# Kernel tuning notes

Hardware: AMD Instinct MI355X
Metric: run time of the kernel (lower is better)

## Reference

```python
import jax, jax.numpy as jnp
import numpy as np

BN_EPS = 1e-5


def _square_distance(src, dst):
    # src: (B,N,3), dst: (B,S,3) -> (B,N,S) squared euclidean distance
    d = -2.0 * jnp.einsum('bnc,bsc->bns', src, dst)
    d += jnp.sum(src * src, -1)[:, :, None]
    d += jnp.sum(dst * dst, -1)[:, None, :]
    return d


def _bn_relu(x, gamma, beta):
    # training-mode BatchNorm1d over (B, C, N): stats over (B, N)
    mean = jnp.mean(x, axis=(0, 2), keepdims=True)
    var = jnp.var(x, axis=(0, 2), keepdims=True)  # biased, as torch uses for normalization
    xhat = (x - mean) * jax.lax.rsqrt(var + BN_EPS)
    return jax.nn.relu(xhat * gamma[None, :, None] + beta[None, :, None])


def setup_inputs() -> dict:
    key = jax.random.key(0)
    ks = jax.random.split(key, 8)
    B, N, S, C1, C2 = 4, 8192, 2048, 128, 256
    inp = {
        'xyz1': jax.random.normal(ks[0], (B, 3, N), jnp.float32),
        'xyz2': jax.random.normal(ks[1], (B, 3, S), jnp.float32),
        'points1': jax.random.normal(ks[2], (B, C1, N), jnp.float32),
        'points2': jax.random.normal(ks[3], (B, C2, S), jnp.float32),
        'w0': jax.random.normal(ks[4], (256, C1 + C2), jnp.float32) * (1.0 / np.sqrt(C1 + C2)),
        'b0': jnp.zeros((256,), jnp.float32),
        'gamma0': jnp.ones((256,), jnp.float32),
        'beta0': jnp.zeros((256,), jnp.float32),
        'w1': jax.random.normal(ks[5], (128, 256), jnp.float32) * (1.0 / np.sqrt(256)),
        'b1': jnp.zeros((128,), jnp.float32),
        'gamma1': jnp.ones((128,), jnp.float32),
        'beta1': jnp.zeros((128,), jnp.float32),
    }
    return inp


def reference(xyz1, xyz2, points1, points2, w0, b0, gamma0, beta0, w1, b1, gamma1, beta1):
    B, _, N = xyz1.shape
    S = xyz2.shape[2]
    xyz1_t = jnp.transpose(xyz1, (0, 2, 1))  # (B,N,3)
    xyz2_t = jnp.transpose(xyz2, (0, 2, 1))  # (B,S,3)
    dist = _square_distance(xyz1_t, xyz2_t)  # (B,N,S)
    neg_d3, idx = jax.lax.top_k(-dist, 3)    # 3 smallest distances
    d3 = -neg_d3                             # (B,N,3)
    dist_recip = 1.0 / (d3 + 1e-8)
    weight = dist_recip / jnp.sum(dist_recip, axis=2, keepdims=True)  # (B,N,3)
    points2_t = jnp.transpose(points2, (0, 2, 1))  # (B,S,C2)
    bidx = jnp.arange(B)[:, None, None]
    neighbor = points2_t[bidx, idx]                 # (B,N,3,C2)
    interp = jnp.sum(neighbor * weight[..., None], axis=2)  # (B,N,C2)
    interp = jnp.transpose(interp, (0, 2, 1))               # (B,C2,N)
    x = jnp.concatenate([points1, interp], axis=1)          # (B,C1+C2,N)
    x = _bn_relu(jnp.einsum('oc,bcn->bon', w0, x) + b0[None, :, None], gamma0, beta0)
    x = _bn_relu(jnp.einsum('oc,bcn->bon', w1, x) + b1[None, :, None], gamma1, beta1)
    return x
```

## Files before the change

### kernel.cpp

```cpp
#include <hip/hip_runtime.h>
#include <hip/hip_bf16.h>

#define BATCH 4
#define NPTS  8192
#define SPTS  2048
#define C1    128
#define C2    256
#define CIN   384
#define H0    256
#define H1    128
#define NSLICE 32

typedef __attribute__((ext_vector_type(8))) short bf16x8;
typedef __attribute__((ext_vector_type(4))) float f32x4;

__device__ __forceinline__ unsigned short f2bf(float x) {
  union { float f; unsigned u; } v; v.f = x;
  unsigned r = v.u + 0x7fff + ((v.u >> 16) & 1);
  return (unsigned short)(r >> 16);
}
__device__ __forceinline__ float bf2f(unsigned short u) {
  union { unsigned u; float f; } v; v.u = ((unsigned)u) << 16; return v.f;
}

__global__ __launch_bounds__(256) void prep_kernel(
    const float* __restrict__ p2, unsigned short* __restrict__ p2tb,
    const float* __restrict__ xyz2, float4* __restrict__ xp,
    const float* __restrict__ w0, const float* __restrict__ w1,
    unsigned short* __restrict__ Wp,
    const float* __restrict__ p1, unsigned short* __restrict__ Xp,
    float* __restrict__ stats) {
  __shared__ unsigned short shmem[64 * 136];
  int bid = blockIdx.x;
  int t = threadIdx.x;

  if (bid < 512) {
    int b = bid >> 7, rem = bid & 127;
    int s0 = (rem >> 2) * 64, c0 = (rem & 3) * 64;
    const float* src = p2 + (size_t)b * C2 * SPTS;
    int ss = t & 63, cseg = t >> 6;
#pragma unroll
    for (int i = 0; i < 16; i++) {
      int cc = cseg + i * 4;
      shmem[ss * 72 + cc] = f2bf(src[(size_t)(c0 + cc) * SPTS + s0 + ss]);
    }
    __syncthreads();
    int s = t >> 2, chunk = t & 3;
    uint4 v0 = *(const uint4*)&shmem[s * 72 + chunk * 16];
    uint4 v1 = *(const uint4*)&shmem[s * 72 + chunk * 16 + 8];
    unsigned short* dst = p2tb + (size_t)b * SPTS * C2 + (size_t)(s0 + s) * C2 + c0 + chunk * 16;
    *(uint4*)dst = v0;
    *(uint4*)(dst + 8) = v1;
  } else if (bid < 1024) {
    int b2 = bid - 512;
    int b = b2 >> 7, n0 = (b2 & 127) * 64;
    int nn = t & 63, c4 = t >> 6;
#pragma unroll
    for (int i = 0; i < 32; i++) {
      int c = i * 4 + c4;
      shmem[nn * 136 + c] = f2bf(p1[((size_t)b * C1 + c) * NPTS + n0 + nn]);
    }
    __syncthreads();
    int n = t >> 2;
#pragma unroll
    for (int j = 0; j < 4; j++) {
      int ch = (t & 3) + j * 4;
      uint4 v = *(const uint4*)&shmem[n * 136 + ch * 8];
      *(uint4*)&Xp[((size_t)b * NPTS + n0 + n) * CIN + ch * 8] = v;
    }
  } else if (bid < 1056) {
    int idx = (bid - 1024) * 256 + t;
    int b = idx >> 11, s = idx & (SPTS - 1);
    const float* x2 = xyz2 + (size_t)b * 3 * SPTS;
    float x = x2[s], y = x2[SPTS + s], z = x2[2 * SPTS + s];
    xp[idx] = make_float4(-2.f * x, -2.f * y, -2.f * z, x * x + y * y + z * z);
  } else if (bid < 1184) {
    int idx = ((bid - 1056) * 256 + t) * 4;
    const float* src = (idx < H0 * CIN) ? (w0 + idx) : (w1 + (idx - H0 * CIN));
    float4 v = *(const float4*)src;
    ushort4 o;
    o.x = f2bf(v.x); o.y = f2bf(v.y); o.z = f2bf(v.z); o.w = f2bf(v.w);
    *(ushort4*)(Wp + idx) = o;
  } else {
    int i4 = ((bid - 1184) * 256 + t) * 4;
    if (i4 < NSLICE * 768) *(float4*)(stats + i4) = make_float4(0.f, 0.f, 0.f, 0.f);
  }
}

#define INS3(d, s, e0, e1, e2, j0, j1, j2)                        \
  {                                                               \
    bool lt0 = (d) < (e0), lt1 = (d) < (e1), lt2 = (d) < (e2);    \
    j2 = lt1 ? (j1) : (lt2 ? (s) : (j2));                         \
    j1 = lt0 ? (j0) : (lt1 ? (s) : (j1));                         \
    j0 = lt0 ? (s) : (j0);                                        \
    e2 = __builtin_amdgcn_fmed3f((d), (e1), (e2));                \
    e1 = __builtin_amdgcn_fmed3f((d), (e0), (e1));                \
    e0 = fminf((d), (e0));                                        \
  }

__global__ __launch_bounds__(1024) void knn_interp_kernel(
    const float* __restrict__ xyz1, const float4* __restrict__ xp,
    const unsigned short* __restrict__ p2tb, unsigned short* __restrict__ Xp) {
  int b = blockIdx.y;
  int t = threadIdx.x;
  int lane = t & 63;
  int w = __builtin_amdgcn_readfirstlane(t >> 6);
  int n = blockIdx.x * 64 + lane;
  const float* x1 = xyz1 + (size_t)b * 3 * NPTS;
  float px = x1[n], py = x1[NPTS + n], pz = x1[2 * NPTS + n];

  const int CHUNK = SPTS / 16;
  int sbase = w * CHUNK;
  const float4* cp = xp + (size_t)b * SPTS + sbase;

  float d0 = 3e38f, d1 = 3e38f, d2 = 3e38f;
  int i0 = 0, i1 = 0, i2 = 0;
#pragma unroll 8
  for (int j = 0; j < CHUNK; j++) {
    float4 c = cp[j];
    float d = fmaf(c.z, pz, fmaf(c.y, py, fmaf(c.x, px, c.w)));
    int s = sbase + j;
    INS3(d, s, d0, d1, d2, i0, i1, i2);
  }

  __shared__ float dsh[16][64][3];
  __shared__ int   ish[16][64][3];
  __shared__ int   widx[64][3];
  __shared__ float wwgt[64][3];
  dsh[w][lane][0] = d0; dsh[w][lane][1] = d1; dsh[w][lane][2] = d2;
  ish[w][lane][0] = i0; ish[w][lane][1] = i1; ish[w][lane][2] = i2;
  __syncthreads();

  if (t < 256) {
    int g = t >> 6, q = t & 63;
    float e0 = 3e38f, e1 = 3e38f, e2 = 3e38f;
    int j0 = 0, j1 = 0, j2 = 0;
#pragma unroll
    for (int c = 0; c < 4; c++) {
#pragma unroll
      for (int k = 0; k < 3; k++) {
        float d = dsh[4 * g + c][q][k];
        int s = ish[4 * g + c][q][k];
        INS3(d, s, e0, e1, e2, j0, j1, j2);
      }
    }
    dsh[4 * g][q][0] = e0; dsh[4 * g][q][1] = e1; dsh[4 * g][q][2] = e2;
    ish[4 * g][q][0] = j0; ish[4 * g][q][1] = j1; ish[4 * g][q][2] = j2;
  }
  __syncthreads();

  if (t < 64) {
    float e0 = 3e38f, e1 = 3e38f, e2 = 3e38f;
    int j0 = 0, j1 = 0, j2 = 0;
#pragma unroll
    for (int c = 0; c < 4; c++) {
#pragma unroll
      for (int k = 0; k < 3; k++) {
        float d = dsh[4 * c][t][k];
        int s = ish[4 * c][t][k];
        INS3(d, s, e0, e1, e2, j0, j1, j2);
      }
    }
    float qq = fmaf(px, px, fmaf(py, py, pz * pz));
    float r0 = 1.f / (e0 + qq + 1e-8f);
    float r1 = 1.f / (e1 + qq + 1e-8f);
    float r2 = 1.f / (e2 + qq + 1e-8f);
    float rs = 1.f / (r0 + r1 + r2);
    widx[t][0] = j0; widx[t][1] = j1; widx[t][2] = j2;
    wwgt[t][0] = r0 * rs; wwgt[t][1] = r1 * rs; wwgt[t][2] = r2 * rs;
  }
  __syncthreads();

  const unsigned short* base = p2tb + (size_t)b * SPTS * C2;
  int c2 = (t & 127) * 2;
  int psub = t >> 7;
  unsigned short* xrow = Xp + ((size_t)b * NPTS + blockIdx.x * 64) * CIN + C1 + c2;
#pragma unroll
  for (int i = 0; i < 8; i++) {
    int pl = psub + i * 8;
    int g0 = widx[pl][0], g1 = widx[pl][1], g2 = widx[pl][2];
    float w0v = wwgt[pl][0], w1v = wwgt[pl][1], w2v = wwgt[pl][2];
    unsigned a0 = *(const unsigned*)(base + (size_t)g0 * C2 + c2);
    unsigned a1 = *(const unsigned*)(base + (size_t)g1 * C2 + c2);
    unsigned a2 = *(const unsigned*)(base + (size_t)g2 * C2 + c2);
    float v0 = w0v * bf2f((unsigned short)a0) + w1v * bf2f((unsigned short)a1) +
               w2v * bf2f((unsigned short)a2);
    float v1 = w0v * bf2f((unsigned short)(a0 >> 16)) + w1v * bf2f((unsigned short)(a1 >> 16)) +
               w2v * bf2f((unsigned short)(a2 >> 16));
    unsigned pk = (unsigned)f2bf(v0) | ((unsigned)f2bf(v1) << 16);
    *(unsigned*)(xrow + (size_t)pl * CIN) = pk;
  }
}

__global__ __launch_bounds__(256) void gemm0_kernel(
    const unsigned short* __restrict__ A, const unsigned short* __restrict__ X,
    const float* __restrict__ bias, unsigned short* __restrict__ Y0,
    float* __restrict__ stats) {
  constexpr int KD = CIN;
  __shared__ unsigned short lds[24576];
  int b = blockIdx.z;
  int n0 = blockIdx.x * 128;
  int o0 = blockIdx.y * 128;
  int t = threadIdx.x;
  int lane = t & 63;
  int w = __builtin_amdgcn_readfirstlane(t >> 6);
  int mhalf = (w & 1) * 64, nhalf = (w >> 1) * 64;
  const unsigned short* Xb = X + (size_t)b * NPTS * KD;
  int rA = lane >> 2;
  int cofs = (lane & 3) * 8;

  auto stage = [&](int buf, int k0) {
#pragma unroll
    for (int q = 0; q < 2; q++) {
      int r0 = w * 32 + q * 16;
      const unsigned short* ga = A + (size_t)(o0 + r0 + rA) * KD + k0 + cofs;
      __builtin_amdgcn_global_load_lds(
          (const __attribute__((address_space(1))) void*)ga,
          (__attribute__((address_space(3))) void*)(lds + buf * 4096 + r0 * 32), 16, 0, 0);
      const unsigned short* gb = Xb + (size_t)(n0 + r0 + rA) * KD + k0 + cofs;
      __builtin_amdgcn_global_load_lds(
          (const __attribute__((address_space(1))) void*)gb,
          (__attribute__((address_space(3))) void*)(lds + 12288 + buf * 4096 + r0 * 32), 16, 0, 0);
    }
  };

  constexpr int NT = KD / 32;
  f32x4 acc[4][4] = {};
  int mi = lane & 15, kq = (lane >> 4) * 8;

  stage(0, 0);
  stage(1, 32);

#pragma unroll
  for (int kt = 0; kt < NT; ++kt) {
    if (kt < NT - 1) asm volatile("s_waitcnt vmcnt(4)" ::: "memory");
    else             asm volatile("s_waitcnt vmcnt(0)" ::: "memory");
    __builtin_amdgcn_s_barrier();
    asm volatile("" ::: "memory");
    __builtin_amdgcn_sched_barrier(0);

    if (kt + 2 < NT) stage((kt + 2) % 3, (kt + 2) * 32);

    const unsigned short* Ac = lds + (kt % 3) * 4096;
    const unsigned short* Bc = lds + 12288 + (kt % 3) * 4096;
    bf16x8 af[4], bfr[4];
#pragma unroll
    for (int i = 0; i < 4; i++) {
      af[i]  = *(const bf16x8*)(Ac + (mhalf + i * 16 + mi) * 32 + kq);
      bfr[i] = *(const bf16x8*)(Bc + (nhalf + i * 16 + mi) * 32 + kq);
    }
#pragma unroll
    for (int mt = 0; mt < 4; mt++)
#pragma unroll
      for (int nt = 0; nt < 4; nt++)
        acc[mt][nt] = __builtin_amdgcn_mfma_f32_16x16x32_bf16(
            af[mt], bfr[nt], acc[mt][nt], 0, 0, 0);
  }

  __syncthreads();

  int slice = ((blockIdx.x << 2) + blockIdx.z) & (NSLICE - 1);
  float* sb = stats + slice * 768;
  float* qb = stats + slice * 768 + 256;

  int rq = (lane >> 4) * 4;
#pragma unroll
  for (int mt = 0; mt < 4; mt++) {
#pragma unroll
    for (int r = 0; r < 4; r++) {
      int ml = mhalf + mt * 16 + rq + r;
      float bv = bias[o0 + ml];
      float ps = 0.f, pq = 0.f;
#pragma unroll
      for (int nt = 0; nt < 4; nt++) {
        int nl = nhalf + nt * 16 + mi;
        float v = acc[mt][nt][r] + bv;
        ps += v; pq += v * v;
        lds[nl * 136 + ml] = f2bf(v);
      }
#pragma unroll
      for (int off = 1; off < 16; off <<= 1) {
        ps += __shfl_xor(ps, off, 16);
        pq += __shfl_xor(pq, off, 16);
      }
      if (mi == 0) {
        atomicAdd(&sb[o0 + ml], ps);
        atomicAdd(&qb[o0 + ml], pq);
      }
    }
  }
  __syncthreads();

  int row = t >> 1, ch0 = (t & 1) * 64;
  unsigned short* Yr = Y0 + ((size_t)b * NPTS + n0 + row) * H0 + o0 + ch0;
#pragma unroll
  for (int j = 0; j < 8; j++) {
    uint4 v = *(const uint4*)&lds[row * 136 + ch0 + j * 8];
    *(uint4*)(Yr + j * 8) = v;
  }
}

__global__ __launch_bounds__(256) void gemm1_kernel(
    const unsigned short* __restrict__ A, const unsigned short* __restrict__ Y0,
    const float* __restrict__ bias, float* __restrict__ out,
    float* __restrict__ stats, const float* __restrict__ gamma0,
    const float* __restrict__ beta0) {
  constexpr int KD = H0;
  __shared__ unsigned short As[2][4096];
  __shared__ unsigned short Bs[2][4096];
  __shared__ float aS[256], sS[256];
  int b = blockIdx.z;
  int n0 = blockIdx.x * 128;
  int t = threadIdx.x;
  int lane = t & 63;
  int w = __builtin_amdgcn_readfirstlane(t >> 6);
  int mhalf = (w & 1) * 64, nhalf = (w >> 1) * 64;
  int rA = lane >> 2;
  int cofs = (lane & 3) * 8;
  const unsigned short* Yb = Y0 + ((size_t)b * NPTS + n0) * KD;

  {
    float ms = 0.f, vs = 0.f;
#pragma unroll 8
    for (int sl = 0; sl < NSLICE; sl++) {
      ms += stats[sl * 768 + t];
      vs += stats[sl * 768 + 256 + t];
    }
    const float inv = 1.f / (float)(BATCH * NPTS);
    float mean = ms * inv;
    float var = vs * inv - mean * mean;
    float ia = gamma0[t] * rsqrtf(var + 1e-5f);
    aS[t] = ia; sS[t] = beta0[t] - mean * ia;
  }
  __syncthreads();

  auto stageA = [&](int buf, int k0) {
#pragma unroll
    for (int q = 0; q < 2; q++) {
      int r0 = w * 32 + q * 16;
      const unsigned short* ga = A + (size_t)(r0 + rA) * KD + k0 + cofs;
      __builtin_amdgcn_global_load_lds(
          (const __attribute__((address_space(1))) void*)ga,
          (__attribute__((address_space(3))) void*)(&As[buf][r0 * 32]), 16, 0, 0);
    }
  };
  bf16x8 br[2];
  auto loadB = [&](int k0) {
#pragma unroll
    for (int q = 0; q < 2; q++) {
      int r0 = w * 32 + q * 16;
      br[q] = *(const bf16x8*)(Yb + (size_t)(r0 + rA) * KD + k0 + cofs);
    }
  };
  auto writeB = [&](int buf, int k0) {
#pragma unroll
    for (int q = 0; q < 2; q++) {
      int r0 = w * 32 + q * 16;
      bf16x8 v = br[q], o;
#pragma unroll
      for (int e = 0; e < 8; e++) {
        float f = bf2f((unsigned short)v[e]);
        f = fmaxf(fmaf(f, aS[k0 + cofs + e], sS[k0 + cofs + e]), 0.f);
        o[e] = (short)f2bf(f);
      }
      *(bf16x8*)(&Bs[buf][(r0 + rA) * 32 + cofs]) = o;
    }
  };

  constexpr int NT = KD / 32;
  f32x4 acc[4][4] = {};
  int mi = lane & 15, kq = (lane >> 4) * 8;

  stageA(0, 0);
  loadB(0);
  int buf = 0;
#pragma unroll
  for (int kt = 0; kt < NT; ++kt) {
    asm volatile("s_waitcnt vmcnt(0)" ::: "memory");
    __builtin_amdgcn_sched_barrier(0);
    writeB(buf, kt * 32);
    asm volatile("s_waitcnt lgkmcnt(0)" ::: "memory");
    asm volatile("s_barrier" ::: "memory");
    __builtin_amdgcn_sched_barrier(0);
    if (kt + 1 < NT) { stageA(buf ^ 1, (kt + 1) * 32); loadB((kt + 1) * 32); }

    bf16x8 af[4], bfr[4];
#pragma unroll
    for (int i = 0; i < 4; i++) {
      af[i]  = *(const bf16x8*)(&As[buf][(mhalf + i * 16 + mi) * 32 + kq]);
      bfr[i] = *(const bf16x8*)(&Bs[buf][(nhalf + i * 16 + mi) * 32 + kq]);
    }
#pragma unroll
    for (int mt = 0; mt < 4; mt++)
#pragma unroll
      for (int nt = 0; nt < 4; nt++)
        acc[mt][nt] = __builtin_amdgcn_mfma_f32_16x16x32_bf16(
            af[mt], bfr[nt], acc[mt][nt], 0, 0, 0);
    buf ^= 1;
  }

  int slice = ((blockIdx.x << 2) + blockIdx.z) & (NSLICE - 1);
  float* sb = stats + slice * 768 + 512;
  float* qb = stats + slice * 768 + 640;
  float* Yo = out + (size_t)b * H1 * NPTS;

  int rq = (lane >> 4) * 4;
#pragma unroll
  for (int mt = 0; mt < 4; mt++) {
#pragma unroll
    for (int r = 0; r < 4; r++) {
      int m = mhalf + mt * 16 + rq + r;
      float bv = bias[m];
      float ps = 0.f, pq = 0.f;
#pragma unroll
      for (int nt = 0; nt < 4; nt++) {
        int n = n0 + nhalf + nt * 16 + mi;
        float v = acc[mt][nt][r] + bv;
        ps += v; pq += v * v;
        Yo[(size_t)m * NPTS + n] = v;
      }
#pragma unroll
      for (int off = 1; off < 16; off <<= 1) {
        ps += __shfl_xor(ps, off, 16);
        pq += __shfl_xor(pq, off, 16);
      }
      if (mi == 0) {
        atomicAdd(&sb[m], ps);
        atomicAdd(&qb[m], pq);
      }
    }
  }
}

__global__ __launch_bounds__(256) void bn_apply_kernel(
    float* __restrict__ Y, const float* __restrict__ stats,
    const float* __restrict__ gamma, const float* __restrict__ beta) {
  __shared__ float sh2[2];
  int idx0 = blockIdx.x * 1024;
  int c = (idx0 >> 13) & (H1 - 1);
  int t = threadIdx.x;
  if (t < 32) {
    float ms = stats[t * 768 + 512 + c];
    float vs = stats[t * 768 + 640 + c];
#pragma unroll
    for (int off = 16; off > 0; off >>= 1) {
      ms += __shfl_down(ms, off, 32);
      vs += __shfl_down(vs, off, 32);
    }
    if (t == 0) {
      const float inv = 1.f / (float)(BATCH * NPTS);
      float mean = ms * inv;
      float var = vs * inv - mean * mean;
      float ia = gamma[c] * rsqrtf(var + 1e-5f);
      sh2[0] = ia; sh2[1] = beta[c] - mean * ia;
    }
  }
  __syncthreads();
  float ia = sh2[0], sh = sh2[1];
  int i = idx0 + t * 4;
  float4 v = *(float4*)(Y + i);
  v.x = fmaxf(v.x * ia + sh, 0.f);
  v.y = fmaxf(v.y * ia + sh, 0.f);
  v.z = fmaxf(v.z * ia + sh, 0.f);
  v.w = fmaxf(v.w * ia + sh, 0.f);
  *(float4*)(Y + i) = v;
}

extern "C" void kernel_launch(void* const* d_in, const int* in_sizes, int n_in,
                              void* d_out, int out_size, void* d_ws, size_t ws_size,
                              hipStream_t stream) {
  const float* xyz1    = (const float*)d_in[0];
  const float* xyz2    = (const float*)d_in[1];
  const float* points1 = (const float*)d_in[2];
  const float* points2 = (const float*)d_in[3];
  const float* w0      = (const float*)d_in[4];
  const float* b0      = (const float*)d_in[5];
  const float* gamma0  = (const float*)d_in[6];
  const float* beta0   = (const float*)d_in[7];
  const float* w1      = (const float*)d_in[8];
  const float* b1      = (const float*)d_in[9];
  const float* gamma1  = (const float*)d_in[10];
  const float* beta1   = (const float*)d_in[11];
  float* out = (float*)d_out;

  char* ws = (char*)d_ws;
  unsigned short* p2tb = (unsigned short*)ws;  ws += (size_t)BATCH * SPTS * C2 * 2;
  unsigned short* Xp = (unsigned short*)ws;    ws += (size_t)BATCH * NPTS * CIN * 2;
  unsigned short* Y0 = (unsigned short*)ws;    ws += (size_t)BATCH * NPTS * H0 * 2;
  unsigned short* Wp = (unsigned short*)ws;    ws += (size_t)(H0 * CIN + H1 * H0) * 2;
  float4* xyz2p = (float4*)(((uintptr_t)ws + 15) & ~(uintptr_t)15);
  ws = (char*)xyz2p + (size_t)BATCH * SPTS * 16;
  float* stats = (float*)ws;                   ws += (size_t)NSLICE * 768 * 4;
  (void)ws_size; (void)in_sizes; (void)n_in; (void)out_size;

  prep_kernel<<<dim3(1208), 256, 0, stream>>>(points2, p2tb, xyz2, xyz2p,
                                              w0, w1, Wp, points1, Xp, stats);
  knn_interp_kernel<<<dim3(NPTS / 64, BATCH), 1024, 0, stream>>>(xyz1, xyz2p, p2tb, Xp);
  gemm0_kernel<<<dim3(NPTS / 128, H0 / 128, BATCH), 256, 0, stream>>>(
      Wp, Xp, b0, Y0, stats);
  gemm1_kernel<<<dim3(NPTS / 128, 1, BATCH), 256, 0, stream>>>(
      Wp + H0 * CIN, Y0, b1, out, stats, gamma0, beta0);
  bn_apply_kernel<<<dim3(BATCH * H1 * NPTS / 1024), 256, 0, stream>>>(
      out, stats, gamma1, beta1);
}
```

Before: 180.8 us.

## Fuse both MLP GEMMs and BN passes into one persistent kernel with grid barriers

The gemm0, gemm1 and bn_apply kernels are replaced by a single persistent kernel of 256 blocks. Each block computes all 256 layer-0 channels for its 128 points and keeps them in LDS instead of writing Y0 to global memory. It then waits at a grid barrier for the BN0 statistics, runs the second GEMM from LDS, and waits at a second grid barrier before applying BN1 and ReLU in registers before the final store. This removes the Y0 round trip, the separate BN pass over the output, and two launches. In exchange it depends on all 256 blocks being co-resident, does atomic spin-waits, reads W1 straight from global memory, and uses fewer blocks than before, which lowers parallelism.

New measurement: 218.8 us. 1.21x slower.

```diff
diff --git a/kernel.cpp b/kernel.cpp
--- a/kernel.cpp
+++ b/kernel.cpp
@@ -10,6 +10,7 @@
 #define H0    256
 #define H1    128
 #define NSLICE 32
+#define GRID_MLP 256
 
 typedef __attribute__((ext_vector_type(8))) short bf16x8;
 typedef __attribute__((ext_vector_type(4))) float f32x4;
@@ -21,6 +22,17 @@
 }
 __device__ __forceinline__ float bf2f(unsigned short u) {
   union { unsigned u; float f; } v; v.u = ((unsigned)u) << 16; return v.f;
+}
+
+__device__ __forceinline__ void grid_barrier(int* bar, int target) {
+  __syncthreads();
+  if (threadIdx.x == 0) {
+    __threadfence();
+    __hip_atomic_fetch_add(bar, 1, __ATOMIC_RELEASE, __HIP_MEMORY_SCOPE_AGENT);
+    while (__hip_atomic_load(bar, __ATOMIC_ACQUIRE, __HIP_MEMORY_SCOPE_AGENT) < target)
+      __builtin_amdgcn_s_sleep(2);
+  }
+  __syncthreads();
 }
 
 __global__ __launch_bounds__(256) void prep_kernel(
@@ -83,7 +95,7 @@
     *(ushort4*)(Wp + idx) = o;
   } else {
     int i4 = ((bid - 1184) * 256 + t) * 4;
-    if (i4 < NSLICE * 768) *(float4*)(stats + i4) = make_float4(0.f, 0.f, 0.f, 0.f);
+    if (i4 < NSLICE * 768 + 16) *(float4*)(stats + i4) = make_float4(0.f, 0.f, 0.f, 0.f);
   }
 }
 
@@ -192,278 +204,228 @@
   }
 }
 
-__global__ __launch_bounds__(256) void gemm0_kernel(
-    const unsigned short* __restrict__ A, const unsigned short* __restrict__ X,
-    const float* __restrict__ bias, unsigned short* __restrict__ Y0,
-    float* __restrict__ stats) {
-  constexpr int KD = CIN;
-  __shared__ unsigned short lds[24576];
-  int b = blockIdx.z;
-  int n0 = blockIdx.x * 128;
-  int o0 = blockIdx.y * 128;
+__global__ __launch_bounds__(256, 1) void fused_mlp_kernel(
+    const unsigned short* __restrict__ Wp, const unsigned short* __restrict__ Xp,
+    const float* __restrict__ bias0, const float* __restrict__ g0,
+    const float* __restrict__ be0, const float* __restrict__ bias1,
+    const float* __restrict__ g1, const float* __restrict__ be1,
+    float* __restrict__ out, float* __restrict__ stats) {
+  __shared__ unsigned short lds[36864];
+  __shared__ float aS0[256], sS0[256], aS1[128], sS1[128];
+  int* gbar = (int*)(stats + NSLICE * 768);
+
+  int bid = blockIdx.x;
+  int b = bid >> 6;
+  int n0 = (bid & 63) * 128;
   int t = threadIdx.x;
   int lane = t & 63;
   int w = __builtin_amdgcn_readfirstlane(t >> 6);
-  int mhalf = (w & 1) * 64, nhalf = (w >> 1) * 64;
-  const unsigned short* Xb = X + (size_t)b * NPTS * KD;
+  int mi = lane & 15, kq = (lane >> 4) * 8;
+  int rq = (lane >> 4) * 4;
   int rA = lane >> 2;
   int cofs = (lane & 3) * 8;
+  int slice = bid & (NSLICE - 1);
+
+  int mq = (w & 1) * 128;
+  int nh = (w >> 1) * 64;
+  const unsigned short* Xb = Xp + ((size_t)b * NPTS + n0) * CIN;
 
   auto stage = [&](int buf, int k0) {
+    unsigned short* dstA = lds + buf * 12288;
+    unsigned short* dstB = dstA + 8192;
+#pragma unroll
+    for (int q = 0; q < 4; q++) {
+      int r0 = w * 64 + q * 16;
+      const unsigned short* ga = Wp + (size_t)(r0 + rA) * CIN + k0 + cofs;
+      __builtin_amdgcn_global_load_lds(
+          (const __attribute__((address_space(1))) void*)ga,
+          (__attribute__((address_space(3))) void*)(dstA + r0 * 32), 16, 0, 0);
+    }
 #pragma unroll
     for (int q = 0; q < 2; q++) {
       int r0 = w * 32 + q * 16;
-      const unsigned short* ga = A + (size_t)(o0 + r0 + rA) * KD + k0 + cofs;
-      __builtin_amdgcn_global_load_lds(
-          (const __attribute__((address_space(1))) void*)ga,
-          (__attribute__((address_space(3))) void*)(lds + buf * 4096 + r0 * 32), 16, 0, 0);
-      const unsigned short* gb = Xb + (size_t)(n0 + r0 + rA) * KD + k0 + cofs;
+      const unsigned short* gb = Xb + (size_t)(r0 + rA) * CIN + k0 + cofs;
       __builtin_amdgcn_global_load_lds(
           (const __attribute__((address_space(1))) void*)gb,
-          (__attribute__((address_space(3))) void*)(lds + 12288 + buf * 4096 + r0 * 32), 16, 0, 0);
+          (__attribute__((address_space(3))) void*)(dstB + r0 * 32), 16, 0, 0);
     }
   };
 
-  constexpr int NT = KD / 32;
-  f32x4 acc[4][4] = {};
-  int mi = lane & 15, kq = (lane >> 4) * 8;
+  constexpr int NT0 = CIN / 32;
+  f32x4 acc[8][4] = {};
 
   stage(0, 0);
   stage(1, 32);
 
 #pragma unroll
-  for (int kt = 0; kt < NT; ++kt) {
-    if (kt < NT - 1) asm volatile("s_waitcnt vmcnt(4)" ::: "memory");
-    else             asm volatile("s_waitcnt vmcnt(0)" ::: "memory");
+  for (int kt = 0; kt < NT0; ++kt) {
+    if (kt < NT0 - 1) asm volatile("s_waitcnt vmcnt(6)" ::: "memory");
+    else              asm volatile("s_waitcnt vmcnt(0)" ::: "memory");
     __builtin_amdgcn_s_barrier();
     asm volatile("" ::: "memory");
     __builtin_amdgcn_sched_barrier(0);
 
-    if (kt + 2 < NT) stage((kt + 2) % 3, (kt + 2) * 32);
-
-    const unsigned short* Ac = lds + (kt % 3) * 4096;
-    const unsigned short* Bc = lds + 12288 + (kt % 3) * 4096;
-    bf16x8 af[4], bfr[4];
-#pragma unroll
-    for (int i = 0; i < 4; i++) {
-      af[i]  = *(const bf16x8*)(Ac + (mhalf + i * 16 + mi) * 32 + kq);
-      bfr[i] = *(const bf16x8*)(Bc + (nhalf + i * 16 + mi) * 32 + kq);
-    }
-#pragma unroll
-    for (int mt = 0; mt < 4; mt++)
-#pragma unroll
-      for (int nt = 0; nt < 4; nt++)
-        acc[mt][nt] = __builtin_amdgcn_mfma_f32_16x16x32_bf16(
-            af[mt], bfr[nt], acc[mt][nt], 0, 0, 0);
-  }
-
-  __syncthreads();
-
-  int slice = ((blockIdx.x << 2) + blockIdx.z) & (NSLICE - 1);
-  float* sb = stats + slice * 768;
-  float* qb = stats + slice * 768 + 256;
-
-  int rq = (lane >> 4) * 4;
-#pragma unroll
-  for (int mt = 0; mt < 4; mt++) {
-#pragma unroll
-    for (int r = 0; r < 4; r++) {
-      int ml = mhalf + mt * 16 + rq + r;
-      float bv = bias[o0 + ml];
-      float ps = 0.f, pq = 0.f;
-#pragma unroll
-      for (int nt = 0; nt < 4; nt++) {
-        int nl = nhalf + nt * 16 + mi;
-        float v = acc[mt][nt][r] + bv;
-        ps += v; pq += v * v;
-        lds[nl * 136 + ml] = f2bf(v);
-      }
-#pragma unroll
-      for (int off = 1; off < 16; off <<= 1) {
-        ps += __shfl_xor(ps, off, 16);
-        pq += __shfl_xor(pq, off, 16);
-      }
-      if (mi == 0) {
-        atomicAdd(&sb[o0 + ml], ps);
-        atomicAdd(&qb[o0 + ml], pq);
-      }
-    }
-  }
-  __syncthreads();
-
-  int row = t >> 1, ch0 = (t & 1) * 64;
-  unsigned short* Yr = Y0 + ((size_t)b * NPTS + n0 + row) * H0 + o0 + ch0;
-#pragma unroll
-  for (int j = 0; j < 8; j++) {
-    uint4 v = *(const uint4*)&lds[row * 136 + ch0 + j * 8];
-    *(uint4*)(Yr + j * 8) = v;
-  }
-}
-
-__global__ __launch_bounds__(256) void gemm1_kernel(
-    const unsigned short* __restrict__ A, const unsigned short* __restrict__ Y0,
-    const float* __restrict__ bias, float* __restrict__ out,
-    float* __restrict__ stats, const float* __restrict__ gamma0,
-    const float* __restrict__ beta0) {
-  constexpr int KD = H0;
-  __shared__ unsigned short As[2][4096];
-  __shared__ unsigned short Bs[2][4096];
-  __shared__ float aS[256], sS[256];
-  int b = blockIdx.z;
-  int n0 = blockIdx.x * 128;
-  int t = threadIdx.x;
-  int lane = t & 63;
-  int w = __builtin_amdgcn_readfirstlane(t >> 6);
-  int mhalf = (w & 1) * 64, nhalf = (w >> 1) * 64;
-  int rA = lane >> 2;
-  int cofs = (lane & 3) * 8;
-  const unsigned short* Yb = Y0 + ((size_t)b * NPTS + n0) * KD;
+    if (kt + 2 < NT0) stage((kt + 2) % 3, (kt + 2) * 32);
+
+    const unsigned short* Ac = lds + (kt % 3) * 12288;
+    const unsigned short* Bc = Ac + 8192;
+    bf16x8 af[8], bfr[4];
+#pragma unroll
+    for (int i = 0; i < 8; i++)
+      af[i] = *(const bf16x8*)(Ac + (mq + i * 16 + mi) * 32 + kq);
+#pragma unroll
+    for (int j = 0; j < 4; j++)
+      bfr[j] = *(const bf16x8*)(Bc + (nh + j * 16 + mi) * 32 + kq);
+#pragma unroll
+    for (int i = 0; i < 8; i++)
+#pragma unroll
+      for (int j = 0; j < 4; j++)
+        acc[i][j] = __builtin_amdgcn_mfma_f32_16x16x32_bf16(
+            af[i], bfr[j], acc[i][j], 0, 0, 0);
+  }
+
+  __syncthreads();
+  unsigned short* yt = lds;
+  {
+    float* sb = stats + slice * 768;
+    float* qb = sb + 256;
+#pragma unroll
+    for (int i = 0; i < 8; i++) {
+#pragma unroll
+      for (int rp = 0; rp < 2; rp++) {
+        int m0 = mq + i * 16 + rq + rp * 2;
+        float bva = bias0[m0], bvb = bias0[m0 + 1];
+        float psA = 0.f, pqA = 0.f, psB = 0.f, pqB = 0.f;
+#pragma unroll
+        for (int j = 0; j < 4; j++) {
+          int n = nh + j * 16 + mi;
+          float va = acc[i][j][rp * 2] + bva;
+          float vb = acc[i][j][rp * 2 + 1] + bvb;
+          psA += va; pqA += va * va; psB += vb; pqB += vb * vb;
+          *(unsigned*)&yt[n * 264 + m0] = (unsigned)f2bf(va) | ((unsigned)f2bf(vb) << 16);
+        }
+#pragma unroll
+        for (int off = 1; off < 16; off <<= 1) {
+          psA += __shfl_xor(psA, off, 16); pqA += __shfl_xor(pqA, off, 16);
+          psB += __shfl_xor(psB, off, 16); pqB += __shfl_xor(pqB, off, 16);
+        }
+        if (mi == 0) {
+          atomicAdd(&sb[m0], psA); atomicAdd(&qb[m0], pqA);
+          atomicAdd(&sb[m0 + 1], psB); atomicAdd(&qb[m0 + 1], pqB);
+        }
+      }
+    }
+  }
+  grid_barrier(gbar, GRID_MLP);
 
   {
     float ms = 0.f, vs = 0.f;
-#pragma unroll 8
+#pragma unroll 4
     for (int sl = 0; sl < NSLICE; sl++) {
-      ms += stats[sl * 768 + t];
-      vs += stats[sl * 768 + 256 + t];
+      ms += __hip_atomic_load(&stats[sl * 768 + t], __ATOMIC_RELAXED, __HIP_MEMORY_SCOPE_AGENT);
+      vs += __hip_atomic_load(&stats[sl * 768 + 256 + t], __ATOMIC_RELAXED, __HIP_MEMORY_SCOPE_AGENT);
     }
     const float inv = 1.f / (float)(BATCH * NPTS);
     float mean = ms * inv;
     float var = vs * inv - mean * mean;
-    float ia = gamma0[t] * rsqrtf(var + 1e-5f);
-    aS[t] = ia; sS[t] = beta0[t] - mean * ia;
-  }
-  __syncthreads();
-
-  auto stageA = [&](int buf, int k0) {
-#pragma unroll
-    for (int q = 0; q < 2; q++) {
-      int r0 = w * 32 + q * 16;
-      const unsigned short* ga = A + (size_t)(r0 + rA) * KD + k0 + cofs;
-      __builtin_amdgcn_global_load_lds(
-          (const __attribute__((address_space(1))) void*)ga,
-          (__attribute__((address_space(3))) void*)(&As[buf][r0 * 32]), 16, 0, 0);
-    }
-  };
-  bf16x8 br[2];
-  auto loadB = [&](int k0) {
-#pragma unroll
-    for (int q = 0; q < 2; q++) {
-      int r0 = w * 32 + q * 16;
-      br[q] = *(const bf16x8*)(Yb + (size_t)(r0 + rA) * KD + k0 + cofs);
-    }
-  };
-  auto writeB = [&](int buf, int k0) {
-#pragma unroll
-    for (int q = 0; q < 2; q++) {
-      int r0 = w * 32 + q * 16;
-      bf16x8 v = br[q], o;
+    float ia = g0[t] * rsqrtf(var + 1e-5f);
+    aS0[t] = ia; sS0[t] = be0[t] - mean * ia;
+  }
+  __syncthreads();
+  {
+    int row = t >> 1, c0 = (t & 1) * 128;
+#pragma unroll
+    for (int jj = 0; jj < 16; jj++) {
+      bf16x8 v = *(bf16x8*)&yt[row * 264 + c0 + jj * 8];
+      bf16x8 o;
 #pragma unroll
       for (int e = 0; e < 8; e++) {
-        float f = bf2f((unsigned short)v[e]);
-        f = fmaxf(fmaf(f, aS[k0 + cofs + e], sS[k0 + cofs + e]), 0.f);
+        int ch = c0 + jj * 8 + e;
+        float f = fmaxf(fmaf(bf2f((unsigned short)v[e]), aS0[ch], sS0[ch]), 0.f);
         o[e] = (short)f2bf(f);
       }
-      *(bf16x8*)(&Bs[buf][(r0 + rA) * 32 + cofs]) = o;
-    }
-  };
-
-  constexpr int NT = KD / 32;
-  f32x4 acc[4][4] = {};
-  int mi = lane & 15, kq = (lane >> 4) * 8;
-
-  stageA(0, 0);
-  loadB(0);
-  int buf = 0;
-#pragma unroll
-  for (int kt = 0; kt < NT; ++kt) {
-    asm volatile("s_waitcnt vmcnt(0)" ::: "memory");
-    __builtin_amdgcn_sched_barrier(0);
-    writeB(buf, kt * 32);
-    asm volatile("s_waitcnt lgkmcnt(0)" ::: "memory");
-    asm volatile("s_barrier" ::: "memory");
-    __builtin_amdgcn_sched_barrier(0);
-    if (kt + 1 < NT) { stageA(buf ^ 1, (kt + 1) * 32); loadB((kt + 1) * 32); }
-
-    bf16x8 af[4], bfr[4];
+      *(bf16x8*)&yt[row * 264 + c0 + jj * 8] = o;
+    }
+  }
+  __syncthreads();
+
+  int mh1 = (w & 1) * 64, nh1 = (w >> 1) * 64;
+  const unsigned short* W1 = Wp + H0 * CIN;
+  f32x4 acc1[4][4] = {};
+#pragma unroll
+  for (int kt = 0; kt < H0 / 32; kt++) {
+    bf16x8 a1[4], b1f[4];
+#pragma unroll
+    for (int i = 0; i < 4; i++)
+      a1[i] = *(const bf16x8*)(W1 + (size_t)(mh1 + i * 16 + mi) * H0 + kt * 32 + kq);
+#pragma unroll
+    for (int j = 0; j < 4; j++)
+      b1f[j] = *(const bf16x8*)&yt[(nh1 + j * 16 + mi) * 264 + kt * 32 + kq];
+#pragma unroll
+    for (int i = 0; i < 4; i++)
+#pragma unroll
+      for (int j = 0; j < 4; j++)
+        acc1[i][j] = __builtin_amdgcn_mfma_f32_16x16x32_bf16(
+            a1[i], b1f[j], acc1[i][j], 0, 0, 0);
+  }
+
+  {
+    float* sb = stats + slice * 768 + 512;
+    float* qb = sb + 128;
 #pragma unroll
     for (int i = 0; i < 4; i++) {
-      af[i]  = *(const bf16x8*)(&As[buf][(mhalf + i * 16 + mi) * 32 + kq]);
-      bfr[i] = *(const bf16x8*)(&Bs[buf][(nhalf + i * 16 + mi) * 32 + kq]);
-    }
-#pragma unroll
-    for (int mt = 0; mt < 4; mt++)
-#pragma unroll
-      for (int nt = 0; nt < 4; nt++)
-        acc[mt][nt] = __builtin_amdgcn_mfma_f32_16x16x32_bf16(
-            af[mt], bfr[nt], acc[mt][nt], 0, 0, 0);
-    buf ^= 1;
-  }
-
-  int slice = ((blockIdx.x << 2) + blockIdx.z) & (NSLICE - 1);
-  float* sb = stats + slice * 768 + 512;
-  float* qb = stats + slice * 768 + 640;
-  float* Yo = out + (size_t)b * H1 * NPTS;
-
-  int rq = (lane >> 4) * 4;
-#pragma unroll
-  for (int mt = 0; mt < 4; mt++) {
-#pragma unroll
-    for (int r = 0; r < 4; r++) {
-      int m = mhalf + mt * 16 + rq + r;
-      float bv = bias[m];
-      float ps = 0.f, pq = 0.f;
-#pragma unroll
-      for (int nt = 0; nt < 4; nt++) {
-        int n = n0 + nhalf + nt * 16 + mi;
-        float v = acc[mt][nt][r] + bv;
-        ps += v; pq += v * v;
-        Yo[(size_t)m * NPTS + n] = v;
-      }
-#pragma unroll
-      for (int off = 1; off < 16; off <<= 1) {
-        ps += __shfl_xor(ps, off, 16);
-        pq += __shfl_xor(pq, off, 16);
-      }
-      if (mi == 0) {
-        atomicAdd(&sb[m], ps);
-        atomicAdd(&qb[m], pq);
-      }
-    }
-  }
-}
-
-__global__ __launch_bounds__(256) void bn_apply_kernel(
-    float* __restrict__ Y, const float* __restrict__ stats,
-    const float* __restrict__ gamma, const float* __restrict__ beta) {
-  __shared__ float sh2[2];
-  int idx0 = blockIdx.x * 1024;
-  int c = (idx0 >> 13) & (H1 - 1);
-  int t = threadIdx.x;
-  if (t < 32) {
-    float ms = stats[t * 768 + 512 + c];
-    float vs = stats[t * 768 + 640 + c];
-#pragma unroll
-    for (int off = 16; off > 0; off >>= 1) {
-      ms += __shfl_down(ms, off, 32);
-      vs += __shfl_down(vs, off, 32);
-    }
-    if (t == 0) {
-      const float inv = 1.f / (float)(BATCH * NPTS);
-      float mean = ms * inv;
-      float var = vs * inv - mean * mean;
-      float ia = gamma[c] * rsqrtf(var + 1e-5f);
-      sh2[0] = ia; sh2[1] = beta[c] - mean * ia;
-    }
-  }
-  __syncthreads();
-  float ia = sh2[0], sh = sh2[1];
-  int i = idx0 + t * 4;
-  float4 v = *(float4*)(Y + i);
-  v.x = fmaxf(v.x * ia + sh, 0.f);
-  v.y = fmaxf(v.y * ia + sh, 0.f);
-  v.z = fmaxf(v.z * ia + sh, 0.f);
-  v.w = fmaxf(v.w * ia + sh, 0.f);
-  *(float4*)(Y + i) = v;
+#pragma unroll
+      for (int r = 0; r < 4; r++) {
+        int m = mh1 + i * 16 + rq + r;
+        float bv = bias1[m];
+        float ps = 0.f, pq = 0.f;
+#pragma unroll
+        for (int j = 0; j < 4; j++) {
+          float v = acc1[i][j][r] + bv;
+          acc1[i][j][r] = v;
+          ps += v; pq += v * v;
+        }
+#pragma unroll
+        for (int off = 1; off < 16; off <<= 1) {
+          ps += __shfl_xor(ps, off, 16);
+          pq += __shfl_xor(pq, off, 16);
+        }
+        if (mi == 0) { atomicAdd(&sb[m], ps); atomicAdd(&qb[m], pq); }
+      }
+    }
+  }
+  grid_barrier(gbar, 2 * GRID_MLP);
+
+  if (t < 128) {
+    float ms = 0.f, vs = 0.f;
+#pragma unroll 4
+    for (int sl = 0; sl < NSLICE; sl++) {
+      ms += __hip_atomic_load(&stats[sl * 768 + 512 + t], __ATOMIC_RELAXED, __HIP_MEMORY_SCOPE_AGENT);
+      vs += __hip_atomic_load(&stats[sl * 768 + 640 + t], __ATOMIC_RELAXED, __HIP_MEMORY_SCOPE_AGENT);
+    }
+    const float inv = 1.f / (float)(BATCH * NPTS);
+    float mean = ms * inv;
+    float var = vs * inv - mean * mean;
+    float ia = g1[t] * rsqrtf(var + 1e-5f);
+    aS1[t] = ia; sS1[t] = be1[t] - mean * ia;
+  }
+  __syncthreads();
+  {
+    float* Yo = out + (size_t)b * H1 * NPTS;
+#pragma unroll
+    for (int i = 0; i < 4; i++) {
+#pragma unroll
+      for (int r = 0; r < 4; r++) {
+        int m = mh1 + i * 16 + rq + r;
+        float ia = aS1[m], sh = sS1[m];
+#pragma unroll
+        for (int j = 0; j < 4; j++) {
+          int n = n0 + nh1 + j * 16 + mi;
+          Yo[(size_t)m * NPTS + n] = fmaxf(fmaf(acc1[i][j][r], ia, sh), 0.f);
+        }
+      }
+    }
+  }
 }
 
 extern "C" void kernel_launch(void* const* d_in, const int* in_sizes, int n_in,
@@ -486,20 +448,15 @@
   char* ws = (char*)d_ws;
   unsigned short* p2tb = (unsigned short*)ws;  ws += (size_t)BATCH * SPTS * C2 * 2;
   unsigned short* Xp = (unsigned short*)ws;    ws += (size_t)BATCH * NPTS * CIN * 2;
-  unsigned short* Y0 = (unsigned short*)ws;    ws += (size_t)BATCH * NPTS * H0 * 2;
   unsigned short* Wp = (unsigned short*)ws;    ws += (size_t)(H0 * CIN + H1 * H0) * 2;
   float4* xyz2p = (float4*)(((uintptr_t)ws + 15) & ~(uintptr_t)15);
   ws = (char*)xyz2p + (size_t)BATCH * SPTS * 16;
-  float* stats = (float*)ws;                   ws += (size_t)NSLICE * 768 * 4;
+  float* stats = (float*)ws;                   ws += (size_t)(NSLICE * 768 + 16) * 4;
   (void)ws_size; (void)in_sizes; (void)n_in; (void)out_size;
 
-  prep_kernel<<<dim3(1208), 256, 0, stream>>>(points2, p2tb, xyz2, xyz2p,
+  prep_kernel<<<dim3(1209), 256, 0, stream>>>(points2, p2tb, xyz2, xyz2p,
                                               w0, w1, Wp, points1, Xp, stats);
   knn_interp_kernel<<<dim3(NPTS / 64, BATCH), 1024, 0, stream>>>(xyz1, xyz2p, p2tb, Xp);
-  gemm0_kernel<<<dim3(NPTS / 128, H0 / 128, BATCH), 256, 0, stream>>>(
-      Wp, Xp, b0, Y0, stats);
-  gemm1_kernel<<<dim3(NPTS / 128, 1, BATCH), 256, 0, stream>>>(
-      Wp + H0 * CIN, Y0, b1, out, stats, gamma0, beta0);
-  bn_apply_kernel<<<dim3(BATCH * H1 * NPTS / 1024), 256, 0, stream>>>(
-      out, stats, gamma1, beta1);
-}
+  fused_mlp_kernel<<<dim3(GRID_MLP), 256, 0, stream>>>(
+      Wp, Xp, b0, gamma0, beta0, b1, gamma1, beta1, out, stats);
+}
```
